# Performance work log

Measured on AMD Instinct MI355X. Metric: run time of the kernel, lower is better.

The kernel has to match this reference:

```python
import jax, jax.numpy as jnp
import numpy as np

NUM_HEADS = 8
OUT_DIM = 32


def setup_inputs() -> dict:
    key = jax.random.key(0)
    ks = jax.random.split(key, 9)
    N, E, IN = 50000, 800000, 256
    HD = NUM_HEADS * OUT_DIM
    s = 1.0 / np.sqrt(IN)
    return {
        "h": jax.random.normal(ks[0], (N, IN), jnp.float32),
        "Wq": jax.random.normal(ks[1], (HD, IN), jnp.float32) * s,
        "bq": jax.random.normal(ks[2], (HD,), jnp.float32) * 0.01,
        "Wk": jax.random.normal(ks[3], (HD, IN), jnp.float32) * s,
        "bk": jax.random.normal(ks[4], (HD,), jnp.float32) * 0.01,
        "Wv": jax.random.normal(ks[5], (HD, IN), jnp.float32) * s,
        "bv": jax.random.normal(ks[6], (HD,), jnp.float32) * 0.01,
        "src": jax.random.randint(ks[7], (E,), 0, N, jnp.int32),
        "dst": jax.random.randint(ks[8], (E,), 0, N, jnp.int32),
    }


def reference(h, Wq, bq, Wk, bk, Wv, bv, src, dst):
    N = h.shape[0]
    H, D = NUM_HEADS, OUT_DIM
    # node projections -> [N, H, D]
    Q = (h @ Wq.T + bq).reshape(N, H, D)
    K = (h @ Wk.T + bk).reshape(N, H, D)
    V = (h @ Wv.T + bv).reshape(N, H, D)
    scale = jnp.asarray(np.sqrt(D), h.dtype)
    # per-edge scores: dot(K[src], Q[dst]) over D -> [E, H]
    score = jnp.exp(jnp.clip((K[src] * Q[dst]).sum(-1) / scale, -5.0, 5.0))
    # segment-softmax denominator over destination nodes -> [N, H]
    z = jax.ops.segment_sum(score, dst, num_segments=N)
    alpha = score / z[dst]  # [E, H]; every edge's dst has z > 0
    # weighted aggregation: sum over in-edges of alpha * V[src] -> [N, H, D]
    wV = jax.ops.segment_sum(V[src] * alpha[:, :, None], dst, num_segments=N)
    return wV
```

## Files before the change

kernel.cpp:

```cpp
#include <hip/hip_runtime.h>
#include <hip/hip_bf16.h>


#define CAP_LOG 6
#define CAP     64

typedef __attribute__((ext_vector_type(8))) short short8;
typedef __attribute__((ext_vector_type(8))) unsigned short ushortx8;
typedef __attribute__((ext_vector_type(4))) unsigned short ushortx4;
typedef __attribute__((ext_vector_type(4))) float floatx4;
typedef __attribute__((ext_vector_type(4))) int intx4;

__device__ __forceinline__ void g2l16(const void* g, void* l) {
    __builtin_amdgcn_global_load_lds(
        (const __attribute__((address_space(1))) unsigned int*)g,
        (__attribute__((address_space(3))) unsigned int*)l, 16, 0, 0);
}

__device__ __forceinline__ float bf2f(unsigned short u) {
    union { unsigned int i; float f; } c; c.i = ((unsigned int)u) << 16; return c.f;
}
__device__ __forceinline__ unsigned short f2bf(float f) {
    __hip_bfloat16 b = __float2bfloat16(f);
    return *reinterpret_cast<unsigned short*>(&b);
}

__device__ __forceinline__ ushortx4 cvt4(floatx4 f) {
    ushortx4 u;
    u.x = f2bf(f.x); u.y = f2bf(f.y); u.z = f2bf(f.z); u.w = f2bf(f.w);
    return u;
}

#define PREP_G 1792

__global__ __launch_bounds__(256) void prep(
    const float* __restrict__ h, unsigned short* __restrict__ hb,
    const float* __restrict__ Wq, const float* __restrict__ Wk, const float* __restrict__ Wv,
    unsigned short* __restrict__ Wb, int* __restrict__ cursor,
    int n4h, int N)
{
    const int bid = blockIdx.x;
    const int tid = threadIdx.x;
    const int gt = bid * 256 + tid;
    const int NT = PREP_G * 256;

    if (bid < 48) {
        const int wstride = 48 * 256;
#pragma unroll
        for (int r = 0; r < 4; r++) {
            int i = r * wstride + bid * 256 + tid;
            int mat = i >> 14, j = i & 16383;
            const floatx4* ws = (const floatx4*)((mat == 0) ? Wq : (mat == 1) ? Wk : Wv);
            ((ushortx4*)Wb)[i] = cvt4(__builtin_nontemporal_load(ws + j));
        }
    } else if (bid < 64) {
        for (int n = (bid - 48) * 256 + tid; n < N; n += 16 * 256)
            cursor[n] = n << CAP_LOG;
    }

    {
        const floatx4* hs = (const floatx4*)h;
        ushortx4* hd = (ushortx4*)hb;
        int i = gt;
        for (; i + 3 * NT < n4h; i += 4 * NT) {
            floatx4 f0 = __builtin_nontemporal_load(hs + i);
            floatx4 f1 = __builtin_nontemporal_load(hs + i + NT);
            floatx4 f2 = __builtin_nontemporal_load(hs + i + 2 * NT);
            floatx4 f3 = __builtin_nontemporal_load(hs + i + 3 * NT);
            hd[i] = cvt4(f0);
            hd[i + NT] = cvt4(f1);
            hd[i + 2 * NT] = cvt4(f2);
            hd[i + 3 * NT] = cvt4(f3);
        }
        for (; i < n4h; i += NT)
            hd[i] = cvt4(__builtin_nontemporal_load(hs + i));
    }
}

#define SCAT_BLOCKS 256

__global__ __launch_bounds__(256) void gemm_scatter(
    const unsigned short* __restrict__ hb, const unsigned short* __restrict__ Wb,
    const float* __restrict__ bq, const float* __restrict__ bk, const float* __restrict__ bv,
    unsigned short* __restrict__ Qb, unsigned short* __restrict__ KV, int N,
    const int* __restrict__ dst, const int* __restrict__ src,
    int* __restrict__ cursor, unsigned short* __restrict__ ssorted, int E, int nb6)
{
    __shared__ unsigned short Ast[2][128 * 32];
    __shared__ unsigned short Bst[2][128 * 32];

    const int bid = blockIdx.x;
    const int tid = threadIdx.x;

    if (bid < SCAT_BLOCKS) {
        const int t = bid * 256 + tid;
        const int nt = SCAT_BLOCKS * 256;
        const int ne4 = E >> 2;
        const intx4* d4 = (const intx4*)dst;
        const intx4* s4 = (const intx4*)src;
        for (int i = t; i < ne4; i += nt) {
            intx4 d = __builtin_nontemporal_load(d4 + i);
            intx4 s = __builtin_nontemporal_load(s4 + i);
            int sl;
            sl = atomicAdd(&cursor[d.x], 1);
            if (sl < ((d.x + 1) << CAP_LOG)) ssorted[sl] = (unsigned short)s.x;
            sl = atomicAdd(&cursor[d.y], 1);
            if (sl < ((d.y + 1) << CAP_LOG)) ssorted[sl] = (unsigned short)s.y;
            sl = atomicAdd(&cursor[d.z], 1);
            if (sl < ((d.z + 1) << CAP_LOG)) ssorted[sl] = (unsigned short)s.z;
            sl = atomicAdd(&cursor[d.w], 1);
            if (sl < ((d.w + 1) << CAP_LOG)) ssorted[sl] = (unsigned short)s.w;
        }
        if (t == 0) {
            for (int e = ne4 * 4; e < E; e++) {
                int d = dst[e];
                int sl = atomicAdd(&cursor[d], 1);
                if (sl < ((d + 1) << CAP_LOG)) ssorted[sl] = (unsigned short)src[e];
            }
        }
        return;
    }

    const int wave = tid >> 6;
    const int lane = tid & 63;
    const int m = lane & 15;
    const int q = lane >> 4;
    const int wr = wave >> 1, wc = wave & 1;

    const int orig = bid - SCAT_BLOCKS;
    const int q8 = nb6 >> 3, r8 = nb6 & 7;
    const int xcd = orig & 7;
    const int wgid = (xcd < r8 ? xcd * (q8 + 1) : r8 * (q8 + 1) + (xcd - r8) * q8)
                     + (orig >> 3);
    const int bx = wgid / 6;
    const int by = wgid % 6;

    const int mbase = bx * 128;
    const int mat = by >> 1;
    const int colbase = (by & 1) * 128;
    const int wrow0 = by * 128;

    const float* bias = (mat == 0) ? bq : (mat == 1) ? bk : bv;

    floatx4 acc[4][4] = {};

    for (int kk = 0; kk < 256; kk += 64) {
#pragma unroll
        for (int c = 0; c < 2; c++) {
#pragma unroll
            for (int t = 0; t < 2; t++) {
                int f = t * 256 + tid;
                int row = f >> 2, kc = f & 3;
                int grow = mbase + row; if (grow > N - 1) grow = N - 1;
                g2l16(hb + (size_t)grow * 256 + kk + c * 32 + kc * 8,
                      Ast[c] + (size_t)(t * 256 + wave * 64) * 8);
            }
#pragma unroll
            for (int t = 0; t < 2; t++) {
                int f = t * 256 + tid;
                int row = f >> 2, kc = f & 3;
                g2l16(Wb + (size_t)(wrow0 + row) * 256 + kk + c * 32 + kc * 8,
                      Bst[c] + (size_t)(t * 256 + wave * 64) * 8);
            }
        }
        __syncthreads();

#pragma unroll
        for (int c = 0; c < 2; c++) {
            short8 a[4], b[4];
#pragma unroll
            for (int i = 0; i < 4; i++) {
                int r = wr * 64 + i * 16 + m;
                a[i] = *(const short8*)&Ast[c][r * 32 + q * 8];
            }
#pragma unroll
            for (int j = 0; j < 4; j++) {
                int cc = wc * 64 + j * 16 + m;
                b[j] = *(const short8*)&Bst[c][cc * 32 + q * 8];
            }
#pragma unroll
            for (int i = 0; i < 4; i++)
#pragma unroll
                for (int j = 0; j < 4; j++)
                    acc[i][j] = __builtin_amdgcn_mfma_f32_16x16x32_bf16(a[i], b[j], acc[i][j], 0, 0, 0);
        }
        __syncthreads();
    }

    float bvj[4];
#pragma unroll
    for (int j = 0; j < 4; j++) bvj[j] = bias[colbase + wc * 64 + j * 16 + m];

    const int col0 = colbase + wc * 64 + m;
#pragma unroll
    for (int i = 0; i < 4; i++) {
#pragma unroll
        for (int r = 0; r < 4; r++) {
            int grow = mbase + wr * 64 + i * 16 + q * 4 + r;
            if (grow < N) {
                if (mat == 0) {
                    unsigned short* op = Qb + (size_t)grow * 256 + col0;
#pragma unroll
                    for (int j = 0; j < 4; j++)
                        __builtin_nontemporal_store(f2bf(acc[i][j][r] + bvj[j]), op + j * 16);
                } else {
                    unsigned short* op = KV + (size_t)grow * 512 + ((mat == 2) ? 256 : 0) + col0;
#pragma unroll
                    for (int j = 0; j < 4; j++)
                        op[j * 16] = f2bf(acc[i][j][r] + bvj[j]);
                }
            }
        }
    }
}

__global__ __launch_bounds__(256) void edge_agg(
    const unsigned short* __restrict__ Qb, const unsigned short* __restrict__ KV,
    const int* __restrict__ cursor, const unsigned short* __restrict__ ssorted,
    float* __restrict__ out, int N)
{
    const int wave = threadIdx.x >> 6;
    const int lane = threadIdx.x & 63;
    const int half = lane >> 5;
    const int hl = lane & 31;
    const int n = blockIdx.x * 4 + wave;
    if (n >= N) return;

    float q[8];
    {
        ushortx8 qu = __builtin_nontemporal_load((const ushortx8*)(Qb + (size_t)n * 256 + hl * 8));
#pragma unroll
        for (int j = 0; j < 8; j++) q[j] = bf2f(qu[j]);
    }

    float acc[8] = {};
    float z = 0.f;
    const int beg = n << CAP_LOG;
    int end = cursor[n];
    const int cap = beg + CAP;
    if (end > cap) end = cap;
    const int len = end - beg;
    const int mid = beg + ((len + 1) >> 1);
    const float scale = 0.17677669529663687f;

    int i = half ? mid : beg;
    const int i1 = half ? end : mid;

    for (; i + 1 < i1; i += 2) {
        int s0 = __builtin_nontemporal_load(ssorted + i);
        int s1 = __builtin_nontemporal_load(ssorted + i + 1);
        const unsigned short* p0 = KV + (size_t)s0 * 512 + hl * 8;
        const unsigned short* p1 = KV + (size_t)s1 * 512 + hl * 8;
        ushortx8 k0 = *(const ushortx8*)p0;        ushortx8 v0 = *(const ushortx8*)(p0 + 256);
        ushortx8 k1 = *(const ushortx8*)p1;        ushortx8 v1 = *(const ushortx8*)(p1 + 256);

        float d0 = 0.f, d1 = 0.f;
#pragma unroll
        for (int j = 0; j < 8; j++) {
            d0 = fmaf(bf2f(k0[j]), q[j], d0);
            d1 = fmaf(bf2f(k1[j]), q[j], d1);
        }
        d0 += __shfl_xor(d0, 1); d0 += __shfl_xor(d0, 2);
        d1 += __shfl_xor(d1, 1); d1 += __shfl_xor(d1, 2);
        float e0 = __expf(fminf(5.f, fmaxf(-5.f, d0 * scale)));
        float e1 = __expf(fminf(5.f, fmaxf(-5.f, d1 * scale)));
        z += e0 + e1;
#pragma unroll
        for (int j = 0; j < 8; j++) {
            acc[j] = fmaf(e0, bf2f(v0[j]), acc[j]);
            acc[j] = fmaf(e1, bf2f(v1[j]), acc[j]);
        }
    }
    for (; i < i1; i++) {
        int s = __builtin_nontemporal_load(ssorted + i);
        const unsigned short* p = KV + (size_t)s * 512 + hl * 8;
        ushortx8 k8 = *(const ushortx8*)p;
        ushortx8 v8 = *(const ushortx8*)(p + 256);
        float d = 0.f;
#pragma unroll
        for (int j = 0; j < 8; j++) d = fmaf(bf2f(k8[j]), q[j], d);
        d += __shfl_xor(d, 1); d += __shfl_xor(d, 2);
        float sc = __expf(fminf(5.f, fmaxf(-5.f, d * scale)));
        z += sc;
#pragma unroll
        for (int j = 0; j < 8; j++) acc[j] = fmaf(sc, bf2f(v8[j]), acc[j]);
    }

    z += __shfl_xor(z, 32);
#pragma unroll
    for (int j = 0; j < 8; j++) acc[j] += __shfl_xor(acc[j], 32);

    if (half == 0) {
        float inv = (z > 0.f) ? 1.f / z : 0.f;
        floatx4 o0, o1;
        o0[0] = acc[0] * inv; o0[1] = acc[1] * inv; o0[2] = acc[2] * inv; o0[3] = acc[3] * inv;
        o1[0] = acc[4] * inv; o1[1] = acc[5] * inv; o1[2] = acc[6] * inv; o1[3] = acc[7] * inv;
        floatx4* op = (floatx4*)(out + (size_t)n * 256 + hl * 8);
        __builtin_nontemporal_store(o0, op);
        __builtin_nontemporal_store(o1, op + 1);
    }
}

extern "C" void kernel_launch(void* const* d_in, const int* in_sizes, int n_in,
                              void* d_out, int out_size, void* d_ws, size_t ws_size,
                              hipStream_t stream) {
    const float* h  = (const float*)d_in[0];
    const float* Wq = (const float*)d_in[1];
    const float* bq = (const float*)d_in[2];
    const float* Wk = (const float*)d_in[3];
    const float* bk = (const float*)d_in[4];
    const float* Wv = (const float*)d_in[5];
    const float* bv = (const float*)d_in[6];
    const int*   src = (const int*)d_in[7];
    const int*   dst = (const int*)d_in[8];
    float* out = (float*)d_out;

    const int N = in_sizes[0] / 256;
    const int E = in_sizes[7];

    size_t off = 0;
    auto alloc = [&](size_t bytes) {
        void* p = (char*)d_ws + off;
        off += (bytes + 255) & ~(size_t)255;
        return p;
    };
    unsigned short* Qb = (unsigned short*)alloc((size_t)N * 256 * 2);
    unsigned short* KV = (unsigned short*)alloc((size_t)N * 512 * 2);
    unsigned short* hb = (unsigned short*)alloc((size_t)N * 256 * 2);
    unsigned short* Wb = (unsigned short*)alloc((size_t)768 * 256 * 2);
    int* cursor   = (int*)alloc((size_t)N * 4);
    unsigned short* ssorted = (unsigned short*)alloc((size_t)N * CAP * 2);

    int n4h = (N * 256) / 4;
    prep<<<PREP_G, 256, 0, stream>>>(h, hb, Wq, Wk, Wv, Wb, cursor, n4h, N);

    int nb6 = ((N + 127) / 128) * 6;
    gemm_scatter<<<SCAT_BLOCKS + nb6, 256, 0, stream>>>(
        hb, Wb, bq, bk, bv, Qb, KV, N, dst, src, cursor, ssorted, E, nb6);

    int ablocks = (N + 3) / 4;
    edge_agg<<<ablocks, 256, 0, stream>>>(Qb, KV, cursor, ssorted, out, N);
}
```

Measured before the change: 293.5 us.

## Fuse fp32-to-bf16 conversion into GEMM loads and drop prep kernel

Removes the separate prep kernel that converted h and the weights to bf16. The GEMM now reads fp32 directly from global memory and converts to bf16 while storing into LDS, replacing the async global_load_lds path. Cursors become per-node counts zeroed by hipMemsetAsync instead of base offsets. The edge aggregation is split into two launches over halves of the nodes. This saves the bf16 intermediate write and reread and one kernel launch. In exchange the GEMM loads twice the bytes through registers and loses the direct-to-LDS loads, and re-reads fp32 h across six column blocks.

After: 316.8 us. 7.9% more time.

```diff
diff --git a/kernel.cpp b/kernel.cpp
--- a/kernel.cpp
+++ b/kernel.cpp
@@ -4,6 +4,7 @@
 
 #define CAP_LOG 6
 #define CAP     64
+#define SCAT_BLOCKS 256
 
 typedef __attribute__((ext_vector_type(8))) short short8;
 typedef __attribute__((ext_vector_type(8))) unsigned short ushortx8;
@@ -11,12 +12,6 @@
 typedef __attribute__((ext_vector_type(4))) float floatx4;
 typedef __attribute__((ext_vector_type(4))) int intx4;
 
-__device__ __forceinline__ void g2l16(const void* g, void* l) {
-    __builtin_amdgcn_global_load_lds(
-        (const __attribute__((address_space(1))) unsigned int*)g,
-        (__attribute__((address_space(3))) unsigned int*)l, 16, 0, 0);
-}
-
 __device__ __forceinline__ float bf2f(unsigned short u) {
     union { unsigned int i; float f; } c; c.i = ((unsigned int)u) << 16; return c.f;
 }
@@ -24,63 +19,16 @@
     __hip_bfloat16 b = __float2bfloat16(f);
     return *reinterpret_cast<unsigned short*>(&b);
 }
-
-__device__ __forceinline__ ushortx4 cvt4(floatx4 f) {
-    ushortx4 u;
-    u.x = f2bf(f.x); u.y = f2bf(f.y); u.z = f2bf(f.z); u.w = f2bf(f.w);
+__device__ __forceinline__ ushortx8 cvt8(floatx4 a, floatx4 b) {
+    ushortx8 u;
+    u[0] = f2bf(a.x); u[1] = f2bf(a.y); u[2] = f2bf(a.z); u[3] = f2bf(a.w);
+    u[4] = f2bf(b.x); u[5] = f2bf(b.y); u[6] = f2bf(b.z); u[7] = f2bf(b.w);
     return u;
 }
 
-#define PREP_G 1792
-
-__global__ __launch_bounds__(256) void prep(
-    const float* __restrict__ h, unsigned short* __restrict__ hb,
+__global__ __launch_bounds__(256) void gemm_scatter(
+    const float* __restrict__ h,
     const float* __restrict__ Wq, const float* __restrict__ Wk, const float* __restrict__ Wv,
-    unsigned short* __restrict__ Wb, int* __restrict__ cursor,
-    int n4h, int N)
-{
-    const int bid = blockIdx.x;
-    const int tid = threadIdx.x;
-    const int gt = bid * 256 + tid;
-    const int NT = PREP_G * 256;
-
-    if (bid < 48) {
-        const int wstride = 48 * 256;
-#pragma unroll
-        for (int r = 0; r < 4; r++) {
-            int i = r * wstride + bid * 256 + tid;
-            int mat = i >> 14, j = i & 16383;
-            const floatx4* ws = (const floatx4*)((mat == 0) ? Wq : (mat == 1) ? Wk : Wv);
-            ((ushortx4*)Wb)[i] = cvt4(__builtin_nontemporal_load(ws + j));
-        }
-    } else if (bid < 64) {
-        for (int n = (bid - 48) * 256 + tid; n < N; n += 16 * 256)
-            cursor[n] = n << CAP_LOG;
-    }
-
-    {
-        const floatx4* hs = (const floatx4*)h;
-        ushortx4* hd = (ushortx4*)hb;
-        int i = gt;
-        for (; i + 3 * NT < n4h; i += 4 * NT) {
-            floatx4 f0 = __builtin_nontemporal_load(hs + i);
-            floatx4 f1 = __builtin_nontemporal_load(hs + i + NT);
-            floatx4 f2 = __builtin_nontemporal_load(hs + i + 2 * NT);
-            floatx4 f3 = __builtin_nontemporal_load(hs + i + 3 * NT);
-            hd[i] = cvt4(f0);
-            hd[i + NT] = cvt4(f1);
-            hd[i + 2 * NT] = cvt4(f2);
-            hd[i + 3 * NT] = cvt4(f3);
-        }
-        for (; i < n4h; i += NT)
-            hd[i] = cvt4(__builtin_nontemporal_load(hs + i));
-    }
-}
-
-#define SCAT_BLOCKS 256
-
-__global__ __launch_bounds__(256) void gemm_scatter(
-    const unsigned short* __restrict__ hb, const unsigned short* __restrict__ Wb,
     const float* __restrict__ bq, const float* __restrict__ bk, const float* __restrict__ bv,
     unsigned short* __restrict__ Qb, unsigned short* __restrict__ KV, int N,
     const int* __restrict__ dst, const int* __restrict__ src,
@@ -103,19 +51,19 @@
             intx4 s = __builtin_nontemporal_load(s4 + i);
             int sl;
             sl = atomicAdd(&cursor[d.x], 1);
-            if (sl < ((d.x + 1) << CAP_LOG)) ssorted[sl] = (unsigned short)s.x;
+            if (sl < CAP) ssorted[(d.x << CAP_LOG) + sl] = (unsigned short)s.x;
             sl = atomicAdd(&cursor[d.y], 1);
-            if (sl < ((d.y + 1) << CAP_LOG)) ssorted[sl] = (unsigned short)s.y;
+            if (sl < CAP) ssorted[(d.y << CAP_LOG) + sl] = (unsigned short)s.y;
             sl = atomicAdd(&cursor[d.z], 1);
-            if (sl < ((d.z + 1) << CAP_LOG)) ssorted[sl] = (unsigned short)s.z;
+            if (sl < CAP) ssorted[(d.z << CAP_LOG) + sl] = (unsigned short)s.z;
             sl = atomicAdd(&cursor[d.w], 1);
-            if (sl < ((d.w + 1) << CAP_LOG)) ssorted[sl] = (unsigned short)s.w;
+            if (sl < CAP) ssorted[(d.w << CAP_LOG) + sl] = (unsigned short)s.w;
         }
         if (t == 0) {
             for (int e = ne4 * 4; e < E; e++) {
                 int d = dst[e];
                 int sl = atomicAdd(&cursor[d], 1);
-                if (sl < ((d + 1) << CAP_LOG)) ssorted[sl] = (unsigned short)src[e];
+                if (sl < CAP) ssorted[(d << CAP_LOG) + sl] = (unsigned short)src[e];
             }
         }
         return;
@@ -138,8 +86,9 @@
     const int mbase = bx * 128;
     const int mat = by >> 1;
     const int colbase = (by & 1) * 128;
-    const int wrow0 = by * 128;
-
+    const int wrowL = (by & 1) * 128;
+
+    const float* Wmat = (mat == 0) ? Wq : (mat == 1) ? Wk : Wv;
     const float* bias = (mat == 0) ? bq : (mat == 1) ? bk : bv;
 
     floatx4 acc[4][4] = {};
@@ -152,15 +101,17 @@
                 int f = t * 256 + tid;
                 int row = f >> 2, kc = f & 3;
                 int grow = mbase + row; if (grow > N - 1) grow = N - 1;
-                g2l16(hb + (size_t)grow * 256 + kk + c * 32 + kc * 8,
-                      Ast[c] + (size_t)(t * 256 + wave * 64) * 8);
+                const floatx4* s4 = (const floatx4*)(h + (size_t)grow * 256 + kk + c * 32 + kc * 8);
+                floatx4 f0 = s4[0], f1 = s4[1];
+                *(ushortx8*)&Ast[c][f * 8] = cvt8(f0, f1);
             }
 #pragma unroll
             for (int t = 0; t < 2; t++) {
                 int f = t * 256 + tid;
                 int row = f >> 2, kc = f & 3;
-                g2l16(Wb + (size_t)(wrow0 + row) * 256 + kk + c * 32 + kc * 8,
-                      Bst[c] + (size_t)(t * 256 + wave * 64) * 8);
+                const floatx4* s4 = (const floatx4*)(Wmat + (size_t)(wrowL + row) * 256 + kk + c * 32 + kc * 8);
+                floatx4 f0 = s4[0], f1 = s4[1];
+                *(ushortx8*)&Bst[c][f * 8] = cvt8(f0, f1);
             }
         }
         __syncthreads();
@@ -217,14 +168,14 @@
 __global__ __launch_bounds__(256) void edge_agg(
     const unsigned short* __restrict__ Qb, const unsigned short* __restrict__ KV,
     const int* __restrict__ cursor, const unsigned short* __restrict__ ssorted,
-    float* __restrict__ out, int N)
+    float* __restrict__ out, int n0, int n1)
 {
     const int wave = threadIdx.x >> 6;
     const int lane = threadIdx.x & 63;
     const int half = lane >> 5;
     const int hl = lane & 31;
-    const int n = blockIdx.x * 4 + wave;
-    if (n >= N) return;
+    const int n = n0 + blockIdx.x * 4 + wave;
+    if (n >= n1) return;
 
     float q[8];
     {
@@ -236,10 +187,9 @@
     float acc[8] = {};
     float z = 0.f;
     const int beg = n << CAP_LOG;
-    int end = cursor[n];
-    const int cap = beg + CAP;
-    if (end > cap) end = cap;
-    const int len = end - beg;
+    int len = cursor[n];
+    if (len > CAP) len = CAP;
+    const int end = beg + len;
     const int mid = beg + ((len + 1) >> 1);
     const float scale = 0.17677669529663687f;
 
@@ -326,18 +276,20 @@
     };
     unsigned short* Qb = (unsigned short*)alloc((size_t)N * 256 * 2);
     unsigned short* KV = (unsigned short*)alloc((size_t)N * 512 * 2);
-    unsigned short* hb = (unsigned short*)alloc((size_t)N * 256 * 2);
-    unsigned short* Wb = (unsigned short*)alloc((size_t)768 * 256 * 2);
     int* cursor   = (int*)alloc((size_t)N * 4);
     unsigned short* ssorted = (unsigned short*)alloc((size_t)N * CAP * 2);
 
-    int n4h = (N * 256) / 4;
-    prep<<<PREP_G, 256, 0, stream>>>(h, hb, Wq, Wk, Wv, Wb, cursor, n4h, N);
+    hipMemsetAsync(cursor, 0, (size_t)N * 4, stream);
 
     int nb6 = ((N + 127) / 128) * 6;
     gemm_scatter<<<SCAT_BLOCKS + nb6, 256, 0, stream>>>(
-        hb, Wb, bq, bk, bv, Qb, KV, N, dst, src, cursor, ssorted, E, nb6);
-
-    int ablocks = (N + 3) / 4;
-    edge_agg<<<ablocks, 256, 0, stream>>>(Qb, KV, cursor, ssorted, out, N);
-}
+        h, Wq, Wk, Wv, bq, bk, bv, Qb, KV, N, dst, src, cursor, ssorted, E, nb6);
+
+    int q2 = (N + 1) / 2;
+    for (int c = 0; c < 2; c++) {
+        int lo = c * q2;
+        if (lo >= N) break;
+        int cnt = (N - lo < q2) ? (N - lo) : q2;
+        edge_agg<<<(cnt + 3) / 4, 256, 0, stream>>>(Qb, KV, cursor, ssorted, out, lo, lo + cnt);
+    }
+}
```
